# Kernel tuning notes

Measured on AMD Instinct MI355X. Metric: run time of the kernel, lower is better.

## Reference

```python
import jax, jax.numpy as jnp
import numpy as np

B, F, CH, HW = 4, 16, 1280, 14
NPATCH = HW * HW            # 196
DIM, HEADS, DH = 1024, 16, 64
INNER = HEADS * DH          # 1024
DEPTH, NCLS = 2, 1
SEQ = 1 + F * NPATCH        # 3137
SCALE = DH ** -0.5


def layernorm(t, g, b):
    m = t.mean(-1, keepdims=True)
    v = ((t - m) ** 2).mean(-1, keepdims=True)
    return (t - m) / jnp.sqrt(v + 1e-5) * g + b


def masked_softmax(sim, mask):
    if mask is not None:
        sim = jnp.where(mask, sim, -jnp.finfo(sim.dtype).max)
    return jax.nn.softmax(sim, axis=-1)


def attention(xn, qkv_w, out_w, out_b, mode, frame_mask, cls_mask):
    # xn: [b, N, dim] (pre-normed). mode: 'time' or 'space'.
    b, N, _ = xn.shape
    qkv = xn @ qkv_w                         # [b, N, 3*inner]
    q, k, v = jnp.split(qkv, 3, axis=-1)
    sh = lambda t: t.reshape(b, N, HEADS, DH).transpose(0, 2, 1, 3).reshape(b * HEADS, N, DH)
    q, k, v = sh(q) * SCALE, sh(k), sh(v)
    # cls token attends to everything
    cls_sim = jnp.einsum('bid,bjd->bij', q[:, :1], k)          # [bh, 1, N]
    cls_out = jnp.einsum('bij,bjd->bid', masked_softmax(cls_sim, cls_mask), v)
    if mode == 'time':
        # (bh) (f n) d -> (bh n) f d
        tb = lambda t: t[:, 1:].reshape(-1, F, NPATCH, DH).transpose(0, 2, 1, 3).reshape(-1, F, DH)
        r, m = NPATCH, frame_mask
    else:
        # (bh) (f n) d -> (bh f) n d
        tb = lambda t: t[:, 1:].reshape(-1, NPATCH, DH)
        r, m = F, None
    q_, k_, v_ = tb(q), tb(k), tb(v)
    ck = jnp.repeat(k[:, :1], r, axis=0)     # broadcast cls k/v as prefix
    cv = jnp.repeat(v[:, :1], r, axis=0)
    k_ = jnp.concatenate([ck, k_], axis=1)
    v_ = jnp.concatenate([cv, v_], axis=1)
    sim = jnp.einsum('bid,bjd->bij', q_, k_)
    out = jnp.einsum('bij,bjd->bid', masked_softmax(sim, m), v_)
    if mode == 'time':
        out = out.reshape(b * HEADS, NPATCH, F, DH).transpose(0, 2, 1, 3).reshape(b * HEADS, F * NPATCH, DH)
    else:
        out = out.reshape(b * HEADS, F * NPATCH, DH)
    out = jnp.concatenate([cls_out, out], axis=1)              # [bh, N, d]
    out = out.reshape(b, HEADS, N, DH).transpose(0, 2, 1, 3).reshape(b, N, INNER)
    return out @ out_w + out_b


def _forward(x, patch_w, patch_b, cls_token, pos_emb,
             t_ng, t_nb, t_qkv, t_ow, t_ob,
             s_ng, s_nb, s_qkv, s_ow, s_ob,
             f_ng, f_nb, f_w1, f_b1, f_w2, f_b2,
             o_ng, o_nb, o_w, o_b, mask, identities_mask):
    b, f, c, h, w = x.shape
    n = h * w
    tokens = x.transpose(0, 1, 3, 4, 2).reshape(b, f * n, c) @ patch_w + patch_b
    xt = jnp.concatenate([jnp.broadcast_to(cls_token[None], (b, 1, DIM)), tokens], axis=1)
    N = xt.shape[1]
    xt = xt + pos_emb[:N]
    # frame mask: [b, f, f+1] -> [(b h n), f, f+1]
    fm = jnp.logical_and(mask[:, None, :], identities_mask)
    fm = jnp.pad(fm, ((0, 0), (0, 0), (1, 0)), constant_values=True)
    frame_mask = jnp.broadcast_to(fm[:, None, None], (b, HEADS, n, f, f + 1)).reshape(b * HEADS * n, f, f + 1)
    # cls mask: [(b h), 1, 1 + f*n]
    cm = jnp.broadcast_to(mask[:, None, :, None], (b, HEADS, f, n)).reshape(b * HEADS, 1, f * n)
    cm = jnp.pad(cm, ((0, 0), (0, 0), (1, 0)), constant_values=True)
    for i in range(DEPTH):
        y = attention(layernorm(xt, t_ng[i], t_nb[i]), t_qkv[i], t_ow[i], t_ob[i], 'time', frame_mask, cm)
        xt = xt + y
        y = attention(layernorm(xt, s_ng[i], s_nb[i]), s_qkv[i], s_ow[i], s_ob[i], 'space', None, cm)
        xt = xt + y
        hh = layernorm(xt, f_ng[i], f_nb[i]) @ f_w1[i] + f_b1[i]
        a, g = jnp.split(hh, 2, axis=-1)
        xt = xt + (a * jax.nn.gelu(g, approximate=False)) @ f_w2[i] + f_b2[i]
    cls = layernorm(xt[:, 0], o_ng, o_nb)
    return cls @ o_w + o_b


def setup_inputs() -> dict:
    key = jax.random.key(0)
    ks = jax.random.split(key, 16)
    rn = lambda k, shp: jax.random.normal(k, shp, dtype=jnp.float32) * 0.02
    return {
        'x': jax.random.normal(ks[0], (B, F, CH, HW, HW), dtype=jnp.float32),
        'mask': jnp.ones((B, F), dtype=bool),
        'identities_mask': jnp.ones((B, F, F), dtype=bool),
        'patch_w': rn(ks[1], (CH, DIM)), 'patch_b': jnp.zeros((DIM,), jnp.float32),
        'cls_token': rn(ks[2], (1, DIM)),
        'pos_emb': rn(ks[3], (SEQ, DIM)),
        't_ng': jnp.ones((DEPTH, DIM), jnp.float32), 't_nb': jnp.zeros((DEPTH, DIM), jnp.float32),
        't_qkv': rn(ks[4], (DEPTH, DIM, 3 * INNER)),
        't_ow': rn(ks[5], (DEPTH, INNER, DIM)), 't_ob': jnp.zeros((DEPTH, DIM), jnp.float32),
        's_ng': jnp.ones((DEPTH, DIM), jnp.float32), 's_nb': jnp.zeros((DEPTH, DIM), jnp.float32),
        's_qkv': rn(ks[6], (DEPTH, DIM, 3 * INNER)),
        's_ow': rn(ks[7], (DEPTH, INNER, DIM)), 's_ob': jnp.zeros((DEPTH, DIM), jnp.float32),
        'f_ng': jnp.ones((DEPTH, DIM), jnp.float32), 'f_nb': jnp.zeros((DEPTH, DIM), jnp.float32),
        'f_w1': rn(ks[8], (DEPTH, DIM, DIM * 8)), 'f_b1': jnp.zeros((DEPTH, DIM * 8), jnp.float32),
        'f_w2': rn(ks[9], (DEPTH, DIM * 4, DIM)), 'f_b2': jnp.zeros((DEPTH, DIM), jnp.float32),
        'o_ng': jnp.ones((DIM,), jnp.float32), 'o_nb': jnp.zeros((DIM,), jnp.float32),
        'o_w': rn(ks[10], (DIM, NCLS)), 'o_b': jnp.zeros((NCLS,), jnp.float32),
    }


def reference(x, mask, identities_mask, patch_w, patch_b, cls_token, pos_emb,
              t_ng, t_nb, t_qkv, t_ow, t_ob,
              s_ng, s_nb, s_qkv, s_ow, s_ob,
              f_ng, f_nb, f_w1, f_b1, f_w2, f_b2,
              o_ng, o_nb, o_w, o_b):
    return _forward(x, patch_w, patch_b, cls_token, pos_emb,
                    t_ng, t_nb, t_qkv, t_ow, t_ob,
                    s_ng, s_nb, s_qkv, s_ow, s_ob,
                    f_ng, f_nb, f_w1, f_b1, f_w2, f_b2,
                    o_ng, o_nb, o_w, o_b, mask, identities_mask)
```

## Files before the change

kernel.cpp:

```cpp
#include <hip/hip_runtime.h>


typedef unsigned short u16;
typedef __bf16 bf16x8 __attribute__((ext_vector_type(8)));
typedef float f32x4 __attribute__((ext_vector_type(4)));
typedef u16 u16x8 __attribute__((ext_vector_type(8)));

#define SEQ   3137
#define ROWS  12548
#define MPAD  12672
#define MPADA 12800
#define NTOK  12544
#define NCC   16
#define CHK   197

__device__ __forceinline__ u16 f2b(float f) {
  union { float f; unsigned u; } v; v.f = f;
  unsigned r = v.u + 0x7FFFu + ((v.u >> 16) & 1u);
  return (u16)(r >> 16);
}
__device__ __forceinline__ float b2f(u16 u) {
  union { unsigned u; float f; } v; v.u = ((unsigned)u) << 16;
  return v.f;
}
__device__ __forceinline__ float gelu_f(float g) {
  return 0.5f * g * (1.0f + erff(g * 0.70710678118654752f));
}
__device__ __forceinline__ bool read_bool(const void* p, int idx) {
  const unsigned* w = (const unsigned*)p;
  unsigned w0 = w[0];
  if (w0 == 1u || w0 == 0u) return ((const int*)p)[idx] != 0;
  if (w0 == 0x3F800000u) return w[idx] != 0;
  return ((const unsigned char*)p)[idx] != 0;
}

typedef const __attribute__((address_space(1))) void GVOID;
typedef __attribute__((address_space(3))) void LVOID;
__device__ __forceinline__ void gload_lds16(const void* g, void* l) {
  __builtin_amdgcn_global_load_lds((GVOID*)g, (LVOID*)l, 16, 0, 0);
}

#define G128_LOOP(KVAL)                                                                  \
  const int K = (KVAL);                                                                  \
  const int NT = K >> 5;                                                                 \
  const int tid  = threadIdx.x;                                                          \
  const int lane = tid & 63, wid = tid >> 6;                                             \
  const int wm = wid >> 1, wn = wid & 1;                                                 \
  const long arow0 = (long)blockIdx.y * 128;                                             \
  const long brow0 = (long)blockIdx.x * 128;                                             \
  const int  s_row = tid >> 2;                                               \
  const int  s_swz = (((tid & 3) ^ ((tid >> 3) & 3)) << 4);                              \
  const char* Ag = (const char*)A + (arow0 + s_row) * (long)K * 2 + s_swz;               \
  const char* Bg = (const char*)Bt + (brow0 + s_row) * (long)K * 2 + s_swz;              \
  auto issue = [&](int t) {                                                              \
    char* d = smem + (t % 3) * 16384 + tid * 16;                                         \
    const long kb = (long)t * 64;                                                        \
    gload_lds16(Ag + kb,                    d);                                          \
    gload_lds16(Ag + kb + (long)64 * K * 2, d + 4096);                                   \
    gload_lds16(Bg + kb,                    d + 8192);                                   \
    gload_lds16(Bg + kb + (long)64 * K * 2, d + 12288);                                  \
  };                                                                                     \
  f32x4 acc[4][4] = {};                                                                  \
  const int rd_row_a = wm * 64 + (lane & 15);                                            \
  const int rd_row_b = wn * 64 + (lane & 15);                                            \
  const int rd_kb    = (lane >> 4) << 4;                                                 \
  const int rxor     = ((lane >> 1) & 3) << 4;                                           \
  issue(0); issue(1);                                                                    \
  for (int t = 0; t < NT; ++t) {                                                         \
    if (t + 1 < NT) asm volatile("s_waitcnt vmcnt(4)" ::: "memory");                     \
    else            asm volatile("s_waitcnt vmcnt(0)" ::: "memory");                     \
    __builtin_amdgcn_sched_barrier(0);                                                   \
    __builtin_amdgcn_s_barrier();                                                        \
    __builtin_amdgcn_sched_barrier(0);                                                   \
    const char* Ab = smem + (t % 3) * 16384;                                             \
    const char* Bb = Ab + 8192;                                                          \
    bf16x8 af[4], bfr[4];                                                                \
    _Pragma("unroll")                                                                    \
    for (int mi = 0; mi < 4; ++mi)                                                       \
      af[mi] = *(const bf16x8*)(Ab + (rd_row_a + mi * 16) * 64 + (rd_kb ^ rxor));        \
    _Pragma("unroll")                                                                    \
    for (int ni = 0; ni < 4; ++ni)                                                       \
      bfr[ni] = *(const bf16x8*)(Bb + (rd_row_b + ni * 16) * 64 + (rd_kb ^ rxor));       \
    __builtin_amdgcn_s_setprio(1);                                                       \
    _Pragma("unroll")                                                                    \
    for (int mi = 0; mi < 4; ++mi)                                                       \
      _Pragma("unroll")                                                                  \
      for (int ni = 0; ni < 4; ++ni)                                                     \
        acc[mi][ni] = __builtin_amdgcn_mfma_f32_16x16x32_bf16(af[mi], bfr[ni],           \
                                                              acc[mi][ni], 0, 0, 0);     \
    __builtin_amdgcn_s_setprio(0);                                                       \
    if (t + 2 < NT) issue(t + 2);                                                        \
  }

template<int MODE>
__global__ __launch_bounds__(256) void gemm_bt(
    const u16* __restrict__ A, const u16* __restrict__ Bt,
    const float* __restrict__ bias,
    float* __restrict__ Cf, u16* __restrict__ Cb,
    int Mact, int N, int Kin)
{
  __shared__ char smem[49152];
  G128_LOOP(Kin)

  const int ccol0 = (int)brow0 + wn * 64 + (lane & 15);
  const int rsub  = (lane >> 4) * 4;
  float bv[4];
#pragma unroll
  for (int ni = 0; ni < 4; ++ni) bv[ni] = bias ? bias[ccol0 + ni * 16] : 0.0f;
#pragma unroll
  for (int mi = 0; mi < 4; ++mi) {
#pragma unroll
    for (int r = 0; r < 4; ++r) {
      long row = arow0 + wm * 64 + mi * 16 + rsub + r;
      if (row < Mact) {
#pragma unroll
        for (int ni = 0; ni < 4; ++ni) {
          float v = acc[mi][ni][r] + bv[ni];
          long idx = row * (long)N + ccol0 + ni * 16;
          if (MODE == 0)      Cf[idx] = v;
          else if (MODE == 1) Cf[idx] += v;
          else                Cb[idx] = f2b(v);
        }
      }
    }
  }
}

__global__ __launch_bounds__(256) void gemm_w1_fused(
    const u16* __restrict__ A, const u16* __restrict__ Bt,
    const float* __restrict__ bias, u16* __restrict__ HACT, int Mact)
{
  __shared__ char smem[49152];
  G128_LOOP(1024)

  float* gx = (float*)smem;
  const int colb  = lane & 15;
  const int rsub  = (lane >> 4) * 4;
  const int cbase = blockIdx.x * 64;
  float bv[4];
#pragma unroll
  for (int ni = 0; ni < 4; ++ni)
    bv[ni] = bias[(wn ? 4096 : 0) + cbase + ni * 16 + colb];

  __syncthreads();
  if (wn == 1) {
#pragma unroll
    for (int mi = 0; mi < 4; ++mi)
#pragma unroll
      for (int r = 0; r < 4; ++r) {
        int rl = mi * 16 + rsub + r;
#pragma unroll
        for (int ni = 0; ni < 4; ++ni)
          gx[(wm * 64 + rl) * 68 + ni * 16 + colb] = acc[mi][ni][r] + bv[ni];
      }
  }
  __syncthreads();
  if (wn == 0) {
#pragma unroll
    for (int mi = 0; mi < 4; ++mi)
#pragma unroll
      for (int r = 0; r < 4; ++r) {
        int rl = mi * 16 + rsub + r;
        long row = arow0 + wm * 64 + rl;
        if (row < Mact) {
#pragma unroll
          for (int ni = 0; ni < 4; ++ni) {
            float a = acc[mi][ni][r] + bv[ni];
            float g = gx[(wm * 64 + rl) * 68 + ni * 16 + colb];
            HACT[row * 4096L + cbase + ni * 16 + colb] = f2b(a * gelu_f(g));
          }
        }
      }
  }
}

__global__ __launch_bounds__(256) void transpose_cvt(
    const float* __restrict__ src, u16* __restrict__ dst,
    int R, int C, long sstride, long dstride)
{
  src += (long)blockIdx.z * sstride;
  dst += (long)blockIdx.z * dstride;
  __shared__ float tile[32][33];
  const int r0 = blockIdx.y * 32, c0 = blockIdx.x * 32;
  const int tx = threadIdx.x & 31, ty = threadIdx.x >> 5;
#pragma unroll
  for (int i = 0; i < 32; i += 8) {
    int r = r0 + ty + i, c = c0 + tx;
    if (r < R && c < C) tile[ty + i][tx] = src[(long)r * C + c];
  }
  __syncthreads();
#pragma unroll
  for (int i = 0; i < 32; i += 8) {
    int c = c0 + ty + i, r = r0 + tx;
    if (c < C && r < R) dst[(long)c * R + r] = f2b(tile[tx][ty + i]);
  }
}

__global__ __launch_bounds__(256) void transpose_w1(
    const float* __restrict__ src, u16* __restrict__ dst)
{
  __shared__ float tile[32][33];
  const int r0 = blockIdx.y * 32, c0 = blockIdx.x * 32;
  const int tx = threadIdx.x & 31, ty = threadIdx.x >> 5;
#pragma unroll
  for (int i = 0; i < 32; i += 8)
    tile[ty + i][tx] = src[(long)(r0 + ty + i) * 8192 + c0 + tx];
  __syncthreads();
#pragma unroll
  for (int i = 0; i < 32; i += 8) {
    int n = c0 + ty + i;
    int np = (n < 4096) ? ((n >> 6) * 128 + (n & 63))
                        : (((n - 4096) >> 6) * 128 + 64 + ((n - 4096) & 63));
    dst[(long)np * 1024 + r0 + tx] = f2b(tile[tx][ty + i]);
  }
}

__global__ __launch_bounds__(256) void build_xt(
    const float* __restrict__ TOK, const float* __restrict__ cls,
    const float* __restrict__ pos, float* __restrict__ XT)
{
  const int row = blockIdx.x, tid = threadIdx.x;
  const int b = row / SEQ, s = row % SEQ;
  float4 p = ((const float4*)(pos + (long)s * 1024))[tid];
  float4 t;
  if (s == 0) t = ((const float4*)cls)[tid];
  else        t = ((const float4*)(TOK + ((long)b * 3136 + (s - 1)) * 1024))[tid];
  float4 r; r.x = t.x + p.x; r.y = t.y + p.y; r.z = t.z + p.z; r.w = t.w + p.w;
  ((float4*)(XT + (long)row * 1024))[tid] = r;
}

__global__ __launch_bounds__(256) void ln_rows(
    const float* __restrict__ X, const float* __restrict__ g,
    const float* __restrict__ b, u16* __restrict__ Y)
{
  const int row = blockIdx.x, tid = threadIdx.x;
  const int lane = tid & 63, wid = tid >> 6;
  float4 x = ((const float4*)(X + (long)row * 1024))[tid];
  float s = x.x + x.y + x.z + x.w;
  float q = x.x * x.x + x.y * x.y + x.z * x.z + x.w * x.w;
#pragma unroll
  for (int o = 32; o; o >>= 1) { s += __shfl_xor(s, o); q += __shfl_xor(q, o); }
  __shared__ float ls[4], lq[4];
  if (lane == 0) { ls[wid] = s; lq[wid] = q; }
  __syncthreads();
  s = ls[0] + ls[1] + ls[2] + ls[3];
  q = lq[0] + lq[1] + lq[2] + lq[3];
  const float mean = s * (1.0f / 1024.0f);
  const float rstd = rsqrtf(q * (1.0f / 1024.0f) - mean * mean + 1e-5f);
  float4 gg = ((const float4*)g)[tid];
  float4 bb = ((const float4*)b)[tid];
  ushort4 o4;
  o4.x = f2b((x.x - mean) * rstd * gg.x + bb.x);
  o4.y = f2b((x.y - mean) * rstd * gg.y + bb.y);
  o4.z = f2b((x.z - mean) * rstd * gg.z + bb.z);
  o4.w = f2b((x.w - mean) * rstd * gg.w + bb.w);
  ((ushort4*)(Y + (long)row * 1024))[tid] = o4;
}

__global__ __launch_bounds__(256) void attn_cls_part(
    const u16* __restrict__ QKV, float* __restrict__ PART, const void* __restrict__ maskp)
{
  const int c = blockIdx.x, bh = blockIdx.y;
  const int b = bh >> 4, h = bh & 15;
  const long rowbase = (long)b * SEQ;
  const int tid = threadIdx.x, lane = tid & 63, w = tid >> 6;
  const int rs = lane >> 3, c8 = lane & 7;
  const int start = c * CHK;
  const int end = (start + CHK < SEQ) ? start + CHK : SEQ;

  float qf[8];
  {
    u16x8 qv = *(const u16x8*)(QKV + rowbase * 3072 + h * 64 + c8 * 8);
#pragma unroll
    for (int i = 0; i < 8; ++i) qf[i] = b2f(qv[i]) * 0.125f;
  }

  float m_run = -3.4e38f, s_run = 0.f;
  float acc[8] = {};

  for (int j8 = start + w * 8; j8 < end; j8 += 32) {
    int j = j8 + rs;
    bool valid = (j < end);
    int jc = valid ? j : (end - 1);
    const u16* kp = QKV + (rowbase + jc) * 3072 + 1024 + h * 64 + c8 * 8;
    u16x8 kv = *(const u16x8*)kp;
    u16x8 vv = *(const u16x8*)(kp + 1024);
    float sim = 0.f;
#pragma unroll
    for (int i = 0; i < 8; ++i) sim += b2f(kv[i]) * qf[i];
    sim += __shfl_xor(sim, 1); sim += __shfl_xor(sim, 2); sim += __shfl_xor(sim, 4);
    bool ok = valid && ((jc == 0) || read_bool(maskp, b * 16 + (jc - 1) / 196));
    float simv = ok ? sim : -3.4e38f;
    float mx = simv;
    mx = fmaxf(mx, __shfl_xor(mx, 8));
    mx = fmaxf(mx, __shfl_xor(mx, 16));
    mx = fmaxf(mx, __shfl_xor(mx, 32));
    float new_m = fmaxf(m_run, mx);
    float scale = __expf(m_run - new_m);
    float p = ok ? __expf(simv - new_m) : 0.f;
    m_run = new_m;
    s_run = s_run * scale + p;
#pragma unroll
    for (int i = 0; i < 8; ++i) acc[i] = acc[i] * scale + p * b2f(vv[i]);
  }
#pragma unroll
  for (int o = 8; o <= 32; o <<= 1) {
    s_run += __shfl_xor(s_run, o);
#pragma unroll
    for (int i = 0; i < 8; ++i) acc[i] += __shfl_xor(acc[i], o);
  }

  __shared__ float sm_m[4], sm_s[4], sm_a[4][64];
  if (lane == 0) { sm_m[w] = m_run; sm_s[w] = s_run; }
  if (rs == 0) {
#pragma unroll
    for (int i = 0; i < 8; ++i) sm_a[w][c8 * 8 + i] = acc[i];
  }
  __syncthreads();
  if (tid < 64) {
    float M = fmaxf(fmaxf(sm_m[0], sm_m[1]), fmaxf(sm_m[2], sm_m[3]));
    float S = 0.f, A = 0.f;
#pragma unroll
    for (int ww = 0; ww < 4; ++ww) {
      float e = __expf(sm_m[ww] - M);
      S += sm_s[ww] * e;
      A += sm_a[ww][tid] * e;
    }
    float* outp = PART + ((long)bh * NCC + c) * 72;
    outp[tid] = A;
    if (tid == 0) { outp[64] = M; outp[65] = S; }
  }
}

__global__ __launch_bounds__(64) void attn_cls_comb(
    const float* __restrict__ PART, u16* __restrict__ ATT)
{
  const int bh = blockIdx.x, b = bh >> 4, h = bh & 15;
  const int d = threadIdx.x;
  float M = -3.4e38f;
#pragma unroll
  for (int c = 0; c < NCC; ++c) M = fmaxf(M, PART[((long)bh * NCC + c) * 72 + 64]);
  float S = 0.f, A = 0.f;
#pragma unroll
  for (int c = 0; c < NCC; ++c) {
    const float* p = PART + ((long)bh * NCC + c) * 72;
    float e = __expf(p[64] - M);
    S += p[65] * e;
    A += p[d] * e;
  }
  ATT[((long)b * SEQ) * 1024 + h * 64 + d] = f2b(A / S);
}

__global__ __launch_bounds__(256) void attn_time(
    const u16* __restrict__ QKV, u16* __restrict__ ATT,
    const void* __restrict__ maskp, const void* __restrict__ idmp)
{
  const int g = blockIdx.x;
  const int n = g % 196;
  const int bh = g / 196;
  const int h = bh & 15, b = bh >> 4;
  const long rowbase = (long)b * SEQ;
  const int tid = threadIdx.x;
  __shared__ float q_s[16][65], k_s[17][65], v_s[17][65], p_s[16][18];
  for (int idx = tid; idx < 16 * 64; idx += 256) {
    int i = idx >> 6, d = idx & 63;
    q_s[i][d] = b2f(QKV[(rowbase + 1 + i * 196 + n) * 3072 + h * 64 + d]) * 0.125f;
  }
  for (int idx = tid; idx < 17 * 64; idx += 256) {
    int j = idx >> 6, d = idx & 63;
    long kr = (j == 0) ? rowbase : (rowbase + 1 + (long)(j - 1) * 196 + n);
    k_s[j][d] = b2f(QKV[kr * 3072 + 1024 + h * 64 + d]);
    v_s[j][d] = b2f(QKV[kr * 3072 + 2048 + h * 64 + d]);
  }
  __syncthreads();
#pragma unroll
  for (int pp = 0; pp < 2; ++pp) {
    int idx = tid + pp * 256;
    if (idx < 272) {
      int i = idx / 17, j = idx % 17;
      float s = 0.f;
      for (int d = 0; d < 64; ++d) s += q_s[i][d] * k_s[j][d];
      bool ok = (j == 0) ||
                (read_bool(maskp, b * 16 + (j - 1)) && read_bool(idmp, (b * 16 + i) * 16 + (j - 1)));
      p_s[i][j] = ok ? s : -3.4e38f;
    }
  }
  __syncthreads();
  if (tid < 16) {
    float m = -3.4e38f;
    for (int j = 0; j < 17; ++j) m = fmaxf(m, p_s[tid][j]);
    float su = 0.f;
    for (int j = 0; j < 17; ++j) { float e = __expf(p_s[tid][j] - m); p_s[tid][j] = e; su += e; }
    float inv = 1.0f / su;
    for (int j = 0; j < 17; ++j) p_s[tid][j] *= inv;
  }
  __syncthreads();
  for (int idx = tid; idx < 1024; idx += 256) {
    int i = idx >> 6, d = idx & 63;
    float o = 0.f;
#pragma unroll
    for (int j = 0; j < 17; ++j) o += p_s[i][j] * v_s[j][d];
    ATT[(rowbase + 1 + i * 196 + n) * 1024 + h * 64 + d] = f2b(o);
  }
}

__global__ __launch_bounds__(256) void attn_space(
    const u16* __restrict__ QKV, u16* __restrict__ ATT)
{
  const int g = blockIdx.x;
  const int fr = g & 15, bh = g >> 4;
  const int h = bh & 15, b = bh >> 4;
  const long rowbase = (long)b * SEQ;
  const long qbase = rowbase + 1 + (long)fr * 196;
  const int tid = threadIdx.x, lane = tid & 63, wid = tid >> 6;

  __shared__ u16 Ks[208][72];
  __shared__ u16 Vt[64][232];
  __shared__ u16 Ps[4][16][232];

  for (int c = tid; c < 197 * 8; c += 256) {
    int row = c >> 3, k8 = c & 7;
    long kr = (row == 0) ? rowbase : (qbase + row - 1);
    *(u16x8*)&Ks[row][k8 * 8] = *(const u16x8*)(QKV + kr * 3072 + 1024 + h * 64 + k8 * 8);
  }
  for (int c = tid; c < 64 * 35; c += 256) {
    int d = c / 35, k = 197 + c % 35;
    Vt[d][k] = 0;
  }
  for (int c = tid; c < 4 * 16 * 24; c += 256) {
    int w = c / (16 * 24), rem = c % (16 * 24);
    Ps[w][rem / 24][208 + rem % 24] = 0;
  }
  for (int c = tid; c < 197 * 64; c += 256) {
    int k = c >> 6, d = c & 63;
    long vr = (k == 0) ? rowbase : (qbase + k - 1);
    Vt[d][k] = QKV[vr * 3072 + 2048 + h * 64 + d];
  }
  __syncthreads();

  const int cl = lane & 15, hi = lane >> 4;
  for (int mt = wid; mt < 13; mt += 4) {
    int qi0 = mt * 16 + cl;
    long qrow = qbase + (qi0 < 196 ? qi0 : 0);
    const u16* qp = QKV + qrow * 3072 + h * 64 + hi * 8;
    bf16x8 af0 = *(const bf16x8*)qp;
    bf16x8 af1 = *(const bf16x8*)(qp + 32);

    f32x4 acc[13];
#pragma unroll
    for (int nt = 0; nt < 13; ++nt) {
      acc[nt] = (f32x4){0.f, 0.f, 0.f, 0.f};
      bf16x8 b0 = *(const bf16x8*)&Ks[nt * 16 + cl][hi * 8];
      acc[nt] = __builtin_amdgcn_mfma_f32_16x16x32_bf16(af0, b0, acc[nt], 0, 0, 0);
      bf16x8 b1 = *(const bf16x8*)&Ks[nt * 16 + cl][32 + hi * 8];
      acc[nt] = __builtin_amdgcn_mfma_f32_16x16x32_bf16(af1, b1, acc[nt], 0, 0, 0);
    }
    float mx[4] = {-3.4e38f, -3.4e38f, -3.4e38f, -3.4e38f};
#pragma unroll
    for (int nt = 0; nt < 13; ++nt) {
      int col = nt * 16 + cl;
#pragma unroll
      for (int r = 0; r < 4; ++r) {
        float s = acc[nt][r] * 0.125f;
        if (col >= 197) s = -3.4e38f;
        acc[nt][r] = s;
        mx[r] = fmaxf(mx[r], s);
      }
    }
#pragma unroll
    for (int r = 0; r < 4; ++r) {
#pragma unroll
      for (int o = 8; o; o >>= 1) mx[r] = fmaxf(mx[r], __shfl_xor(mx[r], o));
    }
    float sum[4] = {0.f, 0.f, 0.f, 0.f};
#pragma unroll
    for (int nt = 0; nt < 13; ++nt) {
      int col = nt * 16 + cl;
#pragma unroll
      for (int r = 0; r < 4; ++r) {
        float p = __expf(acc[nt][r] - mx[r]);
        sum[r] += p;
        Ps[wid][hi * 4 + r][col] = f2b(p);
      }
    }
    float inv[4];
#pragma unroll
    for (int r = 0; r < 4; ++r) {
#pragma unroll
      for (int o = 8; o; o >>= 1) sum[r] += __shfl_xor(sum[r], o);
      inv[r] = 1.0f / sum[r];
    }
    f32x4 ov[4];
#pragma unroll
    for (int dt = 0; dt < 4; ++dt) ov[dt] = (f32x4){0.f, 0.f, 0.f, 0.f};
#pragma unroll
    for (int ks = 0; ks < 7; ++ks) {
      bf16x8 pa = *(const bf16x8*)&Ps[wid][cl][ks * 32 + hi * 8];
#pragma unroll
      for (int dt = 0; dt < 4; ++dt) {
        bf16x8 vb = *(const bf16x8*)&Vt[dt * 16 + cl][ks * 32 + hi * 8];
        ov[dt] = __builtin_amdgcn_mfma_f32_16x16x32_bf16(pa, vb, ov[dt], 0, 0, 0);
      }
    }
#pragma unroll
    for (int r = 0; r < 4; ++r) {
      int qi = mt * 16 + hi * 4 + r;
      if (qi < 196) {
        long orow = (qbase + qi) * 1024 + h * 64;
#pragma unroll
        for (int dt = 0; dt < 4; ++dt)
          ATT[orow + dt * 16 + cl] = f2b(ov[dt][r] * inv[r]);
      }
    }
  }
}

__global__ __launch_bounds__(256) void final_head(
    const float* __restrict__ XT, const float* __restrict__ g,
    const float* __restrict__ b, const float* __restrict__ ow,
    const float* __restrict__ ob, float* __restrict__ out)
{
  const int bb = blockIdx.x, tid = threadIdx.x;
  const int lane = tid & 63, wid = tid >> 6;
  float4 x = ((const float4*)(XT + (long)bb * SEQ * 1024))[tid];
  float s = x.x + x.y + x.z + x.w;
  float q = x.x * x.x + x.y * x.y + x.z * x.z + x.w * x.w;
#pragma unroll
  for (int o = 32; o; o >>= 1) { s += __shfl_xor(s, o); q += __shfl_xor(q, o); }
  __shared__ float ls[4], lq[4], lt[4];
  if (lane == 0) { ls[wid] = s; lq[wid] = q; }
  __syncthreads();
  s = ls[0] + ls[1] + ls[2] + ls[3];
  q = lq[0] + lq[1] + lq[2] + lq[3];
  const float mean = s * (1.0f / 1024.0f);
  const float rstd = rsqrtf(q * (1.0f / 1024.0f) - mean * mean + 1e-5f);
  float4 gg = ((const float4*)g)[tid];
  float4 bv = ((const float4*)b)[tid];
  float4 wv = ((const float4*)ow)[tid];
  float t = ((x.x - mean) * rstd * gg.x + bv.x) * wv.x
          + ((x.y - mean) * rstd * gg.y + bv.y) * wv.y
          + ((x.z - mean) * rstd * gg.z + bv.z) * wv.z
          + ((x.w - mean) * rstd * gg.w + bv.w) * wv.w;
#pragma unroll
  for (int o = 32; o; o >>= 1) t += __shfl_xor(t, o);
  if (lane == 0) lt[wid] = t;
  __syncthreads();
  if (tid == 0) out[bb] = lt[0] + lt[1] + lt[2] + lt[3] + ob[0];
}

extern "C" void kernel_launch(void* const* d_in, const int* in_sizes, int n_in,
                              void* d_out, int out_size, void* d_ws, size_t ws_size,
                              hipStream_t stream) {
  const float* x       = (const float*)d_in[0];
  const void*  maskp   = d_in[1];
  const void*  idmp    = d_in[2];
  const float* patch_w = (const float*)d_in[3];
  const float* patch_b = (const float*)d_in[4];
  const float* cls_tok = (const float*)d_in[5];
  const float* pos_emb = (const float*)d_in[6];
  const float* t_ng = (const float*)d_in[7];
  const float* t_nb = (const float*)d_in[8];
  const float* t_qkv = (const float*)d_in[9];
  const float* t_ow = (const float*)d_in[10];
  const float* t_ob = (const float*)d_in[11];
  const float* s_ng = (const float*)d_in[12];
  const float* s_nb = (const float*)d_in[13];
  const float* s_qkv = (const float*)d_in[14];
  const float* s_ow = (const float*)d_in[15];
  const float* s_ob = (const float*)d_in[16];
  const float* f_ng = (const float*)d_in[17];
  const float* f_nb = (const float*)d_in[18];
  const float* f_w1 = (const float*)d_in[19];
  const float* f_b1 = (const float*)d_in[20];
  const float* f_w2 = (const float*)d_in[21];
  const float* f_b2 = (const float*)d_in[22];
  const float* o_ng = (const float*)d_in[23];
  const float* o_nb = (const float*)d_in[24];
  const float* o_w  = (const float*)d_in[25];
  const float* o_b  = (const float*)d_in[26];
  float* out = (float*)d_out;

  const size_t szXT   = (size_t)ROWS * 1024 * 4;
  const size_t szXNA  = (size_t)MPADA * 1024 * 2;
  const size_t szBIG  = (size_t)MPAD * 4096 * 2;
  const size_t szWBUF = (size_t)8192 * 1024 * 2;
  size_t off = 0;
  auto take = [&](size_t b) { size_t o = off; off += (b + 255) & ~(size_t)255; return o; };
  char* base = (char*)d_ws;
  float* XT  = (float*)(base + take(szXT));
  u16*  XNA  = (u16*)(base + take(szXNA));
  char* BIG  = base + take(szBIG);
  u16*  WBUF = (u16*)(base + take(szWBUF));
  if (off > ws_size) return;

  u16*   QKV  = (u16*)BIG;
  u16*   HACT = (u16*)BIG;
  u16*   Xtr  = (u16*)BIG;
  float* TOK  = (float*)(BIG + (size_t)40 * 1024 * 1024);
  float* PART = (float*)(BIG + (size_t)MPAD * 3072 * 2);

  auto tr = [&](const float* s, u16* d, int R, int C) {
    dim3 gr((C + 31) / 32, (R + 31) / 32, 1);
    transpose_cvt<<<gr, 256, 0, stream>>>(s, d, R, C, 0, 0);
  };

  {
    dim3 gr((196 + 31) / 32, (1280 + 31) / 32, 64);
    transpose_cvt<<<gr, 256, 0, stream>>>(x, Xtr, 1280, 196, 1280L * 196, 196L * 1280);
  }
  tr(patch_w, WBUF, 1280, 1024);
  gemm_bt<0><<<dim3(8, 98), 256, 0, stream>>>(Xtr, WBUF, patch_b, TOK, nullptr, NTOK, 1024, 1280);
  build_xt<<<ROWS, 256, 0, stream>>>(TOK, cls_tok, pos_emb, XT);

  for (int L = 0; L < 2; ++L) {
    tr(t_qkv + (size_t)L * 1024 * 3072, WBUF, 1024, 3072);
    ln_rows<<<ROWS, 256, 0, stream>>>(XT, t_ng + L * 1024, t_nb + L * 1024, XNA);
    gemm_bt<2><<<dim3(24, 99), 256, 0, stream>>>(XNA, WBUF, nullptr, nullptr, QKV, MPAD, 3072, 1024);
    tr(t_ow + (size_t)L * 1024 * 1024, WBUF, 1024, 1024);
    attn_cls_part<<<dim3(NCC, 64), 256, 0, stream>>>(QKV, PART, maskp);
    attn_cls_comb<<<64, 64, 0, stream>>>(PART, XNA);
    attn_time<<<NTOK, 256, 0, stream>>>(QKV, XNA, maskp, idmp);
    gemm_bt<1><<<dim3(8, 99), 256, 0, stream>>>(XNA, WBUF, t_ob + L * 1024, XT, nullptr, ROWS, 1024, 1024);
    tr(s_qkv + (size_t)L * 1024 * 3072, WBUF, 1024, 3072);
    ln_rows<<<ROWS, 256, 0, stream>>>(XT, s_ng + L * 1024, s_nb + L * 1024, XNA);
    gemm_bt<2><<<dim3(24, 99), 256, 0, stream>>>(XNA, WBUF, nullptr, nullptr, QKV, MPAD, 3072, 1024);
    tr(s_ow + (size_t)L * 1024 * 1024, WBUF, 1024, 1024);
    attn_cls_part<<<dim3(NCC, 64), 256, 0, stream>>>(QKV, PART, maskp);
    attn_cls_comb<<<64, 64, 0, stream>>>(PART, XNA);
    attn_space<<<1024, 256, 0, stream>>>(QKV, XNA);
    gemm_bt<1><<<dim3(8, 99), 256, 0, stream>>>(XNA, WBUF, s_ob + L * 1024, XT, nullptr, ROWS, 1024, 1024);
    transpose_w1<<<dim3(256, 32), 256, 0, stream>>>(f_w1 + (size_t)L * 1024 * 8192, WBUF);
    ln_rows<<<ROWS, 256, 0, stream>>>(XT, f_ng + L * 1024, f_nb + L * 1024, XNA);
    gemm_w1_fused<<<dim3(64, 99), 256, 0, stream>>>(XNA, WBUF, f_b1 + L * 8192, HACT, ROWS);
    tr(f_w2 + (size_t)L * 4096 * 1024, WBUF, 4096, 1024);
    gemm_bt<1><<<dim3(8, 99), 256, 0, stream>>>(HACT, WBUF, f_b2 + L * 1024, XT, nullptr, ROWS, 1024, 4096);
  }
  final_head<<<4, 256, 0, stream>>>(XT, o_ng, o_nb, o_w, o_b, out);
}
```

Measured before the change: 2.116 ms.

## Widen GEMM block tile to 128x256 with each wave owning a 128x64 strip

```diff
diff --git a/kernel.cpp b/kernel.cpp
--- a/kernel.cpp
+++ b/kernel.cpp
@@ -44,46 +44,46 @@
   const int K = (KVAL);                                                                  \
   const int NT = K >> 5;                                                                 \
   const int tid  = threadIdx.x;                                                          \
-  const int lane = tid & 63, wid = tid >> 6;                                             \
-  const int wm = wid >> 1, wn = wid & 1;                                                 \
+  const int lane = tid & 63, wid = tid >> 6;                    \
   const long arow0 = (long)blockIdx.y * 128;                                             \
-  const long brow0 = (long)blockIdx.x * 128;                                             \
-  const int  s_row = tid >> 2;                                               \
+  const long brow0 = (long)blockIdx.x * 256;                                             \
+  const int  s_row = tid >> 2;                                                \
   const int  s_swz = (((tid & 3) ^ ((tid >> 3) & 3)) << 4);                              \
   const char* Ag = (const char*)A + (arow0 + s_row) * (long)K * 2 + s_swz;               \
   const char* Bg = (const char*)Bt + (brow0 + s_row) * (long)K * 2 + s_swz;              \
   auto issue = [&](int t) {                                                              \
-    char* d = smem + (t % 3) * 16384 + tid * 16;                                         \
+    char* d = smem + (t % 3) * 24576 + tid * 16;                                         \
     const long kb = (long)t * 64;                                                        \
-    gload_lds16(Ag + kb,                    d);                                          \
-    gload_lds16(Ag + kb + (long)64 * K * 2, d + 4096);                                   \
-    gload_lds16(Bg + kb,                    d + 8192);                                   \
-    gload_lds16(Bg + kb + (long)64 * K * 2, d + 12288);                                  \
+    gload_lds16(Ag + kb,                     d);                                         \
+    gload_lds16(Ag + kb + (long)64  * K * 2, d + 4096);                                  \
+    gload_lds16(Bg + kb,                     d + 8192);                                  \
+    gload_lds16(Bg + kb + (long)64  * K * 2, d + 12288);                                 \
+    gload_lds16(Bg + kb + (long)128 * K * 2, d + 16384);                                 \
+    gload_lds16(Bg + kb + (long)192 * K * 2, d + 20480);                                 \
   };                                                                                     \
-  f32x4 acc[4][4] = {};                                                                  \
-  const int rd_row_a = wm * 64 + (lane & 15);                                            \
-  const int rd_row_b = wn * 64 + (lane & 15);                                            \
-  const int rd_kb    = (lane >> 4) << 4;                                                 \
-  const int rxor     = ((lane >> 1) & 3) << 4;                                           \
+  f32x4 acc[8][4] = {};                                                                  \
+  const int frow  = lane & 15;                                                           \
+  const int rd_kb = (lane >> 4) << 4;                                                    \
+  const int rxor  = ((lane >> 1) & 3) << 4;                                              \
   issue(0); issue(1);                                                                    \
   for (int t = 0; t < NT; ++t) {                                                         \
-    if (t + 1 < NT) asm volatile("s_waitcnt vmcnt(4)" ::: "memory");                     \
+    if (t + 1 < NT) asm volatile("s_waitcnt vmcnt(6)" ::: "memory");                     \
     else            asm volatile("s_waitcnt vmcnt(0)" ::: "memory");                     \
     __builtin_amdgcn_sched_barrier(0);                                                   \
     __builtin_amdgcn_s_barrier();                                                        \
     __builtin_amdgcn_sched_barrier(0);                                                   \
-    const char* Ab = smem + (t % 3) * 16384;                                             \
+    const char* Ab = smem + (t % 3) * 24576;                                             \
     const char* Bb = Ab + 8192;                                                          \
-    bf16x8 af[4], bfr[4];                                                                \
+    bf16x8 af[8], bfr[4];                                                                \
     _Pragma("unroll")                                                                    \
-    for (int mi = 0; mi < 4; ++mi)                                                       \
-      af[mi] = *(const bf16x8*)(Ab + (rd_row_a + mi * 16) * 64 + (rd_kb ^ rxor));        \
+    for (int mi = 0; mi < 8; ++mi)                                                       \
+      af[mi] = *(const bf16x8*)(Ab + (mi * 16 + frow) * 64 + (rd_kb ^ rxor));            \
     _Pragma("unroll")                                                                    \
     for (int ni = 0; ni < 4; ++ni)                                                       \
-      bfr[ni] = *(const bf16x8*)(Bb + (rd_row_b + ni * 16) * 64 + (rd_kb ^ rxor));       \
+      bfr[ni] = *(const bf16x8*)(Bb + (wid * 64 + ni * 16 + frow) * 64 + (rd_kb ^ rxor));\
     __builtin_amdgcn_s_setprio(1);                                                       \
     _Pragma("unroll")                                                                    \
-    for (int mi = 0; mi < 4; ++mi)                                                       \
+    for (int mi = 0; mi < 8; ++mi)                                                       \
       _Pragma("unroll")                                                                  \
       for (int ni = 0; ni < 4; ++ni)                                                     \
         acc[mi][ni] = __builtin_amdgcn_mfma_f32_16x16x32_bf16(af[mi], bfr[ni],           \
@@ -93,25 +93,25 @@
   }
 
 template<int MODE>
-__global__ __launch_bounds__(256) void gemm_bt(
+__global__ __launch_bounds__(256, 2) void gemm_bt(
     const u16* __restrict__ A, const u16* __restrict__ Bt,
     const float* __restrict__ bias,
     float* __restrict__ Cf, u16* __restrict__ Cb,
     int Mact, int N, int Kin)
 {
-  __shared__ char smem[49152];
+  __shared__ char smem[73728];
   G128_LOOP(Kin)
 
-  const int ccol0 = (int)brow0 + wn * 64 + (lane & 15);
+  const int ccol0 = (int)brow0 + wid * 64 + frow;
   const int rsub  = (lane >> 4) * 4;
   float bv[4];
 #pragma unroll
   for (int ni = 0; ni < 4; ++ni) bv[ni] = bias ? bias[ccol0 + ni * 16] : 0.0f;
 #pragma unroll
-  for (int mi = 0; mi < 4; ++mi) {
+  for (int mi = 0; mi < 8; ++mi) {
 #pragma unroll
     for (int r = 0; r < 4; ++r) {
-      long row = arow0 + wm * 64 + mi * 16 + rsub + r;
+      long row = arow0 + mi * 16 + rsub + r;
       if (row < Mact) {
 #pragma unroll
         for (int ni = 0; ni < 4; ++ni) {
@@ -126,48 +126,48 @@
   }
 }
 
-__global__ __launch_bounds__(256) void gemm_w1_fused(
+__global__ __launch_bounds__(256, 2) void gemm_w1_fused(
     const u16* __restrict__ A, const u16* __restrict__ Bt,
     const float* __restrict__ bias, u16* __restrict__ HACT, int Mact)
 {
-  __shared__ char smem[49152];
+  __shared__ char smem[73728];
   G128_LOOP(1024)
 
   float* gx = (float*)smem;
-  const int colb  = lane & 15;
+  const int p     = wid >> 1;
+  const int cbase = blockIdx.x * 128 + p * 64;
   const int rsub  = (lane >> 4) * 4;
-  const int cbase = blockIdx.x * 64;
   float bv[4];
 #pragma unroll
   for (int ni = 0; ni < 4; ++ni)
-    bv[ni] = bias[(wn ? 4096 : 0) + cbase + ni * 16 + colb];
-
-  __syncthreads();
-  if (wn == 1) {
-#pragma unroll
-    for (int mi = 0; mi < 4; ++mi)
+    bv[ni] = bias[((wid & 1) ? 4096 : 0) + cbase + ni * 16 + frow];
+
+  __syncthreads();
+  if (wid & 1) {
+#pragma unroll
+    for (int mi = 0; mi < 8; ++mi)
 #pragma unroll
       for (int r = 0; r < 4; ++r) {
         int rl = mi * 16 + rsub + r;
 #pragma unroll
         for (int ni = 0; ni < 4; ++ni)
-          gx[(wm * 64 + rl) * 68 + ni * 16 + colb] = acc[mi][ni][r] + bv[ni];
+          gx[(p * 128 + rl) * 68 + ni * 16 + frow] = acc[mi][ni][r] + bv[ni];
       }
   }
   __syncthreads();
-  if (wn == 0) {
-#pragma unroll
-    for (int mi = 0; mi < 4; ++mi)
+  if (!(wid & 1)) {
+#pragma unroll
+    for (int mi = 0; mi < 8; ++mi)
 #pragma unroll
       for (int r = 0; r < 4; ++r) {
         int rl = mi * 16 + rsub + r;
-        long row = arow0 + wm * 64 + rl;
+        long row = arow0 + rl;
         if (row < Mact) {
 #pragma unroll
           for (int ni = 0; ni < 4; ++ni) {
             float a = acc[mi][ni][r] + bv[ni];
-            float g = gx[(wm * 64 + rl) * 68 + ni * 16 + colb];
-            HACT[row * 4096L + cbase + ni * 16 + colb] = f2b(a * gelu_f(g));
+            float g = gx[(p * 128 + rl) * 68 + ni * 16 + frow];
+            HACT[row * 4096L + cbase + ni * 16 + frow] = f2b(a * gelu_f(g));
           }
         }
       }
@@ -609,31 +609,31 @@
     transpose_cvt<<<gr, 256, 0, stream>>>(x, Xtr, 1280, 196, 1280L * 196, 196L * 1280);
   }
   tr(patch_w, WBUF, 1280, 1024);
-  gemm_bt<0><<<dim3(8, 98), 256, 0, stream>>>(Xtr, WBUF, patch_b, TOK, nullptr, NTOK, 1024, 1280);
+  gemm_bt<0><<<dim3(4, 98), 256, 0, stream>>>(Xtr, WBUF, patch_b, TOK, nullptr, NTOK, 1024, 1280);
   build_xt<<<ROWS, 256, 0, stream>>>(TOK, cls_tok, pos_emb, XT);
 
   for (int L = 0; L < 2; ++L) {
     tr(t_qkv + (size_t)L * 1024 * 3072, WBUF, 1024, 3072);
     ln_rows<<<ROWS, 256, 0, stream>>>(XT, t_ng + L * 1024, t_nb + L * 1024, XNA);
-    gemm_bt<2><<<dim3(24, 99), 256, 0, stream>>>(XNA, WBUF, nullptr, nullptr, QKV, MPAD, 3072, 1024);
+    gemm_bt<2><<<dim3(12, 99), 256, 0, stream>>>(XNA, WBUF, nullptr, nullptr, QKV, MPAD, 3072, 1024);
     tr(t_ow + (size_t)L * 1024 * 1024, WBUF, 1024, 1024);
     attn_cls_part<<<dim3(NCC, 64), 256, 0, stream>>>(QKV, PART, maskp);
     attn_cls_comb<<<64, 64, 0, stream>>>(PART, XNA);
     attn_time<<<NTOK, 256, 0, stream>>>(QKV, XNA, maskp, idmp);
-    gemm_bt<1><<<dim3(8, 99), 256, 0, stream>>>(XNA, WBUF, t_ob + L * 1024, XT, nullptr, ROWS, 1024, 1024);
+    gemm_bt<1><<<dim3(4, 99), 256, 0, stream>>>(XNA, WBUF, t_ob + L * 1024, XT, nullptr, ROWS, 1024, 1024);
     tr(s_qkv + (size_t)L * 1024 * 3072, WBUF, 1024, 3072);
     ln_rows<<<ROWS, 256, 0, stream>>>(XT, s_ng + L * 1024, s_nb + L * 1024, XNA);
-    gemm_bt<2><<<dim3(24, 99), 256, 0, stream>>>(XNA, WBUF, nullptr, nullptr, QKV, MPAD, 3072, 1024);
+    gemm_bt<2><<<dim3(12, 99), 256, 0, stream>>>(XNA, WBUF, nullptr, nullptr, QKV, MPAD, 3072, 1024);
     tr(s_ow + (size_t)L * 1024 * 1024, WBUF, 1024, 1024);
     attn_cls_part<<<dim3(NCC, 64), 256, 0, stream>>>(QKV, PART, maskp);
     attn_cls_comb<<<64, 64, 0, stream>>>(PART, XNA);
     attn_space<<<1024, 256, 0, stream>>>(QKV, XNA);
-    gemm_bt<1><<<dim3(8, 99), 256, 0, stream>>>(XNA, WBUF, s_ob + L * 1024, XT, nullptr, ROWS, 1024, 1024);
+    gemm_bt<1><<<dim3(4, 99), 256, 0, stream>>>(XNA, WBUF, s_ob + L * 1024, XT, nullptr, ROWS, 1024, 1024);
     transpose_w1<<<dim3(256, 32), 256, 0, stream>>>(f_w1 + (size_t)L * 1024 * 8192, WBUF);
     ln_rows<<<ROWS, 256, 0, stream>>>(XT, f_ng + L * 1024, f_nb + L * 1024, XNA);
-    gemm_w1_fused<<<dim3(64, 99), 256, 0, stream>>>(XNA, WBUF, f_b1 + L * 8192, HACT, ROWS);
+    gemm_w1_fused<<<dim3(32, 99), 256, 0, stream>>>(XNA, WBUF, f_b1 + L * 8192, HACT, ROWS);
     tr(f_w2 + (size_t)L * 4096 * 1024, WBUF, 4096, 1024);
-    gemm_bt<1><<<dim3(8, 99), 256, 0, stream>>>(HACT, WBUF, f_b2 + L * 1024, XT, nullptr, ROWS, 1024, 4096);
+    gemm_bt<1><<<dim3(4, 99), 256, 0, stream>>>(HACT, WBUF, f_b2 + L * 1024, XT, nullptr, ROWS, 1024, 4096);
   }
   final_head<<<4, 256, 0, stream>>>(XT, o_ng, o_nb, o_w, o_b, out);
 }
```

Measured after the change: 2.080 ms. Within noise of the previous version (-1.7%).

## Widen generic GEMM tile to 128x256 with per-wave 128x64 subtiles

Applied to the files above, without the earlier changes.

```diff
diff --git a/kernel.cpp b/kernel.cpp
--- a/kernel.cpp
+++ b/kernel.cpp
@@ -40,7 +40,59 @@
   __builtin_amdgcn_global_load_lds((GVOID*)g, (LVOID*)l, 16, 0, 0);
 }
 
-#define G128_LOOP(KVAL)                                                                  \
+#define GLOOP_WIDE(KVAL)                                                                 \
+  const int K = (KVAL);                                                                  \
+  const int NT = K >> 5;                                                                 \
+  const int tid  = threadIdx.x;                                                          \
+  const int lane = tid & 63, wid = tid >> 6;                    \
+  const long arow0 = (long)blockIdx.y * 128;                                             \
+  const long brow0 = (long)blockIdx.x * 256;                                             \
+  const int  s_row = tid >> 2;                                                \
+  const int  s_swz = (((tid & 3) ^ ((tid >> 3) & 3)) << 4);                              \
+  const char* Ag = (const char*)A + (arow0 + s_row) * (long)K * 2 + s_swz;               \
+  const char* Bg = (const char*)Bt + (brow0 + s_row) * (long)K * 2 + s_swz;              \
+  auto issue = [&](int t) {                                                              \
+    char* d = smem + (t % 3) * 24576 + tid * 16;                                         \
+    const long kb = (long)t * 64;                                                        \
+    gload_lds16(Ag + kb,                     d);                                         \
+    gload_lds16(Ag + kb + (long)64  * K * 2, d + 4096);                                  \
+    gload_lds16(Bg + kb,                     d + 8192);                                  \
+    gload_lds16(Bg + kb + (long)64  * K * 2, d + 12288);                                 \
+    gload_lds16(Bg + kb + (long)128 * K * 2, d + 16384);                                 \
+    gload_lds16(Bg + kb + (long)192 * K * 2, d + 20480);                                 \
+  };                                                                                     \
+  f32x4 acc[8][4] = {};                                                                  \
+  const int frow  = lane & 15;                                                           \
+  const int rd_kb = (lane >> 4) << 4;                                                    \
+  const int rxor  = ((lane >> 1) & 3) << 4;                                              \
+  issue(0); issue(1);                                                                    \
+  for (int t = 0; t < NT; ++t) {                                                         \
+    if (t + 1 < NT) asm volatile("s_waitcnt vmcnt(6)" ::: "memory");                     \
+    else            asm volatile("s_waitcnt vmcnt(0)" ::: "memory");                     \
+    __builtin_amdgcn_sched_barrier(0);                                                   \
+    __builtin_amdgcn_s_barrier();                                                        \
+    __builtin_amdgcn_sched_barrier(0);                                                   \
+    const char* Ab = smem + (t % 3) * 24576;                                             \
+    const char* Bb = Ab + 8192;                                                          \
+    bf16x8 af[8], bfr[4];                                                                \
+    _Pragma("unroll")                                                                    \
+    for (int mi = 0; mi < 8; ++mi)                                                       \
+      af[mi] = *(const bf16x8*)(Ab + (mi * 16 + frow) * 64 + (rd_kb ^ rxor));            \
+    _Pragma("unroll")                                                                    \
+    for (int ni = 0; ni < 4; ++ni)                                                       \
+      bfr[ni] = *(const bf16x8*)(Bb + (wid * 64 + ni * 16 + frow) * 64 + (rd_kb ^ rxor));\
+    __builtin_amdgcn_s_setprio(1);                                                       \
+    _Pragma("unroll")                                                                    \
+    for (int mi = 0; mi < 8; ++mi)                                                       \
+      _Pragma("unroll")                                                                  \
+      for (int ni = 0; ni < 4; ++ni)                                                     \
+        acc[mi][ni] = __builtin_amdgcn_mfma_f32_16x16x32_bf16(af[mi], bfr[ni],           \
+                                                              acc[mi][ni], 0, 0, 0);     \
+    __builtin_amdgcn_s_setprio(0);                                                       \
+    if (t + 2 < NT) issue(t + 2);                                                        \
+  }
+
+#define GLOOP_SQ(KVAL)                                                                   \
   const int K = (KVAL);                                                                  \
   const int NT = K >> 5;                                                                 \
   const int tid  = threadIdx.x;                                                          \
@@ -48,7 +100,7 @@
   const int wm = wid >> 1, wn = wid & 1;                                                 \
   const long arow0 = (long)blockIdx.y * 128;                                             \
   const long brow0 = (long)blockIdx.x * 128;                                             \
-  const int  s_row = tid >> 2;                                               \
+  const int  s_row = tid >> 2;                                                           \
   const int  s_swz = (((tid & 3) ^ ((tid >> 3) & 3)) << 4);                              \
   const char* Ag = (const char*)A + (arow0 + s_row) * (long)K * 2 + s_swz;               \
   const char* Bg = (const char*)Bt + (brow0 + s_row) * (long)K * 2 + s_swz;              \
@@ -93,25 +145,25 @@
   }
 
 template<int MODE>
-__global__ __launch_bounds__(256) void gemm_bt(
+__global__ __launch_bounds__(256, 2) void gemm_bt(
     const u16* __restrict__ A, const u16* __restrict__ Bt,
     const float* __restrict__ bias,
     float* __restrict__ Cf, u16* __restrict__ Cb,
     int Mact, int N, int Kin)
 {
-  __shared__ char smem[49152];
-  G128_LOOP(Kin)
-
-  const int ccol0 = (int)brow0 + wn * 64 + (lane & 15);
+  __shared__ char smem[73728];
+  GLOOP_WIDE(Kin)
+
+  const int ccol0 = (int)brow0 + wid * 64 + frow;
   const int rsub  = (lane >> 4) * 4;
   float bv[4];
 #pragma unroll
   for (int ni = 0; ni < 4; ++ni) bv[ni] = bias ? bias[ccol0 + ni * 16] : 0.0f;
 #pragma unroll
-  for (int mi = 0; mi < 4; ++mi) {
+  for (int mi = 0; mi < 8; ++mi) {
 #pragma unroll
     for (int r = 0; r < 4; ++r) {
-      long row = arow0 + wm * 64 + mi * 16 + rsub + r;
+      long row = arow0 + mi * 16 + rsub + r;
       if (row < Mact) {
 #pragma unroll
         for (int ni = 0; ni < 4; ++ni) {
@@ -131,7 +183,7 @@
     const float* __restrict__ bias, u16* __restrict__ HACT, int Mact)
 {
   __shared__ char smem[49152];
-  G128_LOOP(1024)
+  GLOOP_SQ(1024)
 
   float* gx = (float*)smem;
   const int colb  = lane & 15;
@@ -609,31 +661,31 @@
     transpose_cvt<<<gr, 256, 0, stream>>>(x, Xtr, 1280, 196, 1280L * 196, 196L * 1280);
   }
   tr(patch_w, WBUF, 1280, 1024);
-  gemm_bt<0><<<dim3(8, 98), 256, 0, stream>>>(Xtr, WBUF, patch_b, TOK, nullptr, NTOK, 1024, 1280);
+  gemm_bt<0><<<dim3(4, 98), 256, 0, stream>>>(Xtr, WBUF, patch_b, TOK, nullptr, NTOK, 1024, 1280);
   build_xt<<<ROWS, 256, 0, stream>>>(TOK, cls_tok, pos_emb, XT);
 
   for (int L = 0; L < 2; ++L) {
     tr(t_qkv + (size_t)L * 1024 * 3072, WBUF, 1024, 3072);
     ln_rows<<<ROWS, 256, 0, stream>>>(XT, t_ng + L * 1024, t_nb + L * 1024, XNA);
-    gemm_bt<2><<<dim3(24, 99), 256, 0, stream>>>(XNA, WBUF, nullptr, nullptr, QKV, MPAD, 3072, 1024);
+    gemm_bt<2><<<dim3(12, 99), 256, 0, stream>>>(XNA, WBUF, nullptr, nullptr, QKV, MPAD, 3072, 1024);
     tr(t_ow + (size_t)L * 1024 * 1024, WBUF, 1024, 1024);
     attn_cls_part<<<dim3(NCC, 64), 256, 0, stream>>>(QKV, PART, maskp);
     attn_cls_comb<<<64, 64, 0, stream>>>(PART, XNA);
     attn_time<<<NTOK, 256, 0, stream>>>(QKV, XNA, maskp, idmp);
-    gemm_bt<1><<<dim3(8, 99), 256, 0, stream>>>(XNA, WBUF, t_ob + L * 1024, XT, nullptr, ROWS, 1024, 1024);
+    gemm_bt<1><<<dim3(4, 99), 256, 0, stream>>>(XNA, WBUF, t_ob + L * 1024, XT, nullptr, ROWS, 1024, 1024);
     tr(s_qkv + (size_t)L * 1024 * 3072, WBUF, 1024, 3072);
     ln_rows<<<ROWS, 256, 0, stream>>>(XT, s_ng + L * 1024, s_nb + L * 1024, XNA);
-    gemm_bt<2><<<dim3(24, 99), 256, 0, stream>>>(XNA, WBUF, nullptr, nullptr, QKV, MPAD, 3072, 1024);
+    gemm_bt<2><<<dim3(12, 99), 256, 0, stream>>>(XNA, WBUF, nullptr, nullptr, QKV, MPAD, 3072, 1024);
     tr(s_ow + (size_t)L * 1024 * 1024, WBUF, 1024, 1024);
     attn_cls_part<<<dim3(NCC, 64), 256, 0, stream>>>(QKV, PART, maskp);
     attn_cls_comb<<<64, 64, 0, stream>>>(PART, XNA);
     attn_space<<<1024, 256, 0, stream>>>(QKV, XNA);
-    gemm_bt<1><<<dim3(8, 99), 256, 0, stream>>>(XNA, WBUF, s_ob + L * 1024, XT, nullptr, ROWS, 1024, 1024);
+    gemm_bt<1><<<dim3(4, 99), 256, 0, stream>>>(XNA, WBUF, s_ob + L * 1024, XT, nullptr, ROWS, 1024, 1024);
     transpose_w1<<<dim3(256, 32), 256, 0, stream>>>(f_w1 + (size_t)L * 1024 * 8192, WBUF);
     ln_rows<<<ROWS, 256, 0, stream>>>(XT, f_ng + L * 1024, f_nb + L * 1024, XNA);
     gemm_w1_fused<<<dim3(64, 99), 256, 0, stream>>>(XNA, WBUF, f_b1 + L * 8192, HACT, ROWS);
     tr(f_w2 + (size_t)L * 4096 * 1024, WBUF, 4096, 1024);
-    gemm_bt<1><<<dim3(8, 99), 256, 0, stream>>>(HACT, WBUF, f_b2 + L * 1024, XT, nullptr, ROWS, 1024, 4096);
+    gemm_bt<1><<<dim3(4, 99), 256, 0, stream>>>(HACT, WBUF, f_b2 + L * 1024, XT, nullptr, ROWS, 1024, 4096);
   }
   final_head<<<4, 256, 0, stream>>>(XT, o_ng, o_nb, o_w, o_b, out);
 }
```

Result: faster. 1.984 ms (-6.2%).
